# Kernel optimization log

Hardware: AMD Instinct MI355X
Metric: run time of the kernel (lower is better)

## Reference

```python
import jax, jax.numpy as jnp
import numpy as np

N = 100000   # nodes
E = 800000   # edges
H = 256      # hidden_dim == input_dim
L = 3        # num_layers
G = 64       # graphs in batch


def setup_inputs() -> dict:
    key = jax.random.key(0)
    ks = jax.random.split(key, 16)
    s = 0.05
    inp = {
        'x': jax.random.normal(ks[0], (N, H), jnp.float32),
        'edge_index': jax.random.randint(ks[1], (2, E), 0, N, dtype=jnp.int32),
        'batch': jnp.sort(jax.random.randint(ks[2], (N,), 0, G, dtype=jnp.int32)),
        'Ws': jax.random.normal(ks[3], (L, H, H), jnp.float32) * s,
        'Wn': jax.random.normal(ks[4], (L, H, H), jnp.float32) * s,
        'bs': jnp.zeros((L, H), jnp.float32),
        'att_w': jax.random.normal(ks[5], (H, 1), jnp.float32) * s,
        'att_b': jnp.zeros((1,), jnp.float32),
        'ne_W1': jax.random.normal(ks[6], (H, H // 2), jnp.float32) * s,
        'ne_b1': jnp.zeros((H // 2,), jnp.float32),
        'ne_W2': jax.random.normal(ks[7], (H // 2, 1), jnp.float32) * s,
        'ne_b2': jnp.zeros((1,), jnp.float32),
        'nd_W1': jax.random.normal(ks[8], (H, H // 2), jnp.float32) * s,
        'nd_b1': jnp.zeros((H // 2,), jnp.float32),
        'nd_W2': jax.random.normal(ks[9], (H // 2, 1), jnp.float32) * s,
        'nd_b2': jnp.zeros((1,), jnp.float32),
    }
    return inp


def reference(x, edge_index, batch, Ws, Wn, bs, att_w, att_b,
              ne_W1, ne_b1, ne_W2, ne_b2, nd_W1, nd_b1, nd_W2, nd_b2):
    src, dst = edge_index[0], edge_index[1]
    n = x.shape[0]
    # in-degree for mean aggregation (clamped to avoid div-by-zero)
    deg = jax.ops.segment_sum(jnp.ones(src.shape[0], x.dtype), dst, num_segments=n)
    deg = jnp.maximum(deg, 1.0)[:, None]                    # [N,1]
    # GNN encoder: SAGE-mean layers, ReLU (dropout identity at eval)
    h = x
    for l in range(Ws.shape[0]):
        msg = jax.ops.segment_sum(h[src], dst, num_segments=n) / deg  # [N,H]
        h = jax.nn.relu(h @ Ws[l] + msg @ Wn[l] + bs[l])
    # attention pooling: per-graph softmax over node scores
    s = (h @ att_w + att_b)[:, 0]                           # [N]
    m = jax.ops.segment_max(s, batch, num_segments=G)
    e = jnp.exp(s - m[batch])
    denom = jax.ops.segment_sum(e, batch, num_segments=G)
    alpha = (e / denom[batch])[:, None]                     # [N,1]
    g = jax.ops.segment_sum(alpha * h, batch, num_segments=G)  # [G,H]
    # heads: Linear-ReLU-(Dropout)-Linear
    graph_logits = jax.nn.relu(g @ ne_W1 + ne_b1) @ ne_W2 + ne_b2  # [G,1]
    node_logits = jax.nn.relu(h @ nd_W1 + nd_b1) @ nd_W2 + nd_b2  # [N,1]
    return (graph_logits, node_logits)
```

## Files before the change

kernel.cpp:

```cpp
#include <hip/hip_runtime.h>
#include <hip/hip_bf16.h>

#define HID 256
#define HHALF 128

typedef unsigned short u16;
typedef __attribute__((ext_vector_type(8))) short bf16x8;
typedef __attribute__((ext_vector_type(4))) float f32x4;

__device__ __forceinline__ float bf2f(unsigned int u) {
    unsigned int x = (u & 0xffffu) << 16;
    union { unsigned int i; float f; } c; c.i = x; return c.f;
}
__device__ __forceinline__ float lof(unsigned u) {
    union { unsigned i; float f; } c; c.i = u << 16; return c.f;
}
__device__ __forceinline__ float hif(unsigned u) {
    union { unsigned i; float f; } c; c.i = u & 0xffff0000u; return c.f;
}
__device__ __forceinline__ u16 f2bf(float f) {
    __hip_bfloat16 h = __float2bfloat16(f);
    union { __hip_bfloat16 h; u16 u; } c; c.h = h; return c.u;
}

__device__ __forceinline__ void gload16(const u16* g, u16* l) {
    __builtin_amdgcn_global_load_lds(
        (const __attribute__((address_space(1))) void*)g,
        (__attribute__((address_space(3))) void*)l, 16, 0, 0);
}

__device__ __forceinline__ int lbound(const int* __restrict__ a, int n, int key) {
    int lo = 0, hi = n;
    while (lo < hi) {
        int mid = (lo + hi) >> 1;
        if (a[mid] < key) lo = mid + 1; else hi = mid;
    }
    return lo;
}

__global__ void k_count(const int* __restrict__ dst, int* __restrict__ cnt, int E) {
    int i = blockIdx.x * blockDim.x + threadIdx.x;
    if (i < E) atomicAdd(&cnt[dst[i]], 1);
}

__global__ void k_scan_block(const int* __restrict__ cnt, int* __restrict__ bsum, int n) {
    __shared__ int sd[256];
    int tid = threadIdx.x;
    int i = blockIdx.x * 256 + tid;
    int v = (i < n) ? cnt[i] : 0;
    sd[tid] = v; __syncthreads();
    for (int s = 128; s > 0; s >>= 1) {
        if (tid < s) sd[tid] += sd[tid + s];
        __syncthreads();
    }
    if (tid == 0) bsum[blockIdx.x] = sd[0];
}

__global__ void k_scan_top(int* __restrict__ bsum, int nb) {
    __shared__ int sd[512];
    int t = threadIdx.x;
    int v = (t < nb) ? bsum[t] : 0;
    sd[t] = v; __syncthreads();
    for (int s = 1; s < 512; s <<= 1) {
        int x = (t >= s) ? sd[t - s] : 0;
        __syncthreads();
        sd[t] += x;
        __syncthreads();
    }
    if (t < nb) bsum[t] = sd[t] - v;
}

__global__ void k_scan_down(const int* __restrict__ cnt, const int* __restrict__ boff,
                            int* __restrict__ row_off, int n, int total) {
    __shared__ int sd[256];
    int tid = threadIdx.x;
    int i = blockIdx.x * 256 + tid;
    int v = (i < n) ? cnt[i] : 0;
    sd[tid] = v; __syncthreads();
    for (int s = 1; s < 256; s <<= 1) {
        int x = (tid >= s) ? sd[tid - s] : 0;
        __syncthreads();
        sd[tid] += x;
        __syncthreads();
    }
    if (i < n) row_off[i] = boff[blockIdx.x] + sd[tid] - v;
    if (i == 0) row_off[n] = total;
}

__global__ void k_scatter(const int* __restrict__ src, const int* __restrict__ dst,
                          const int* __restrict__ row_off, int* __restrict__ cnt,
                          int* __restrict__ col, int E) {
    int i = blockIdx.x * blockDim.x + threadIdx.x;
    if (i < E) {
        int d = dst[i];
        int p = atomicSub(&cnt[d], 1) - 1;
        col[row_off[d] + p] = src[i];
    }
}

__global__ void k_prep(const float* __restrict__ x, u16* __restrict__ xb, int xtotal4,
                       const float* __restrict__ Ws, const float* __restrict__ Wn,
                       const float* __restrict__ ndW1,
                       u16* __restrict__ WsT, u16* __restrict__ WnT,
                       u16* __restrict__ ndW1T, int L) {
    int idx = blockIdx.x * 256 + threadIdx.x;
    if (idx < xtotal4) {
        float4 v = *(const float4*)&x[(size_t)idx * 4];
        uint2 p;
        p.x = (unsigned)f2bf(v.x) | ((unsigned)f2bf(v.y) << 16);
        p.y = (unsigned)f2bf(v.z) | ((unsigned)f2bf(v.w) << 16);
        *(uint2*)&xb[(size_t)idx * 4] = p;
        return;
    }
    int widx = idx - xtotal4;
    int mat = widx >> 16;
    if (mat >= 2 * L + 1) return;
    int r = widx & 65535;
    int k = r >> 8, c = r & 255;
    if (mat < L) {
        WsT[(size_t)mat * 65536 + c * 256 + k] = f2bf(Ws[(size_t)mat * 65536 + k * 256 + c]);
    } else if (mat < 2 * L) {
        int l = mat - L;
        WnT[(size_t)l * 65536 + c * 256 + k] = f2bf(Wn[(size_t)l * 65536 + k * 256 + c]);
    } else {
        if (c < HHALF) ndW1T[c * 256 + k] = f2bf(ndW1[k * HHALF + c]);
    }
}

__global__ __launch_bounds__(256) void k_agg(
    const u16* __restrict__ h, const int* __restrict__ row_off,
    const int* __restrict__ col, u16* __restrict__ msg, int n) {
    int node = blockIdx.x * 4 + (threadIdx.x >> 6);
    if (node >= n) return;
    int lane = threadIdx.x & 63;
    int half = lane >> 5;
    int t = lane & 31;
    int s0 = row_off[node], s1 = row_off[node + 1];
    float a0 = 0.f, a1 = 0.f, a2 = 0.f, a3 = 0.f;
    float a4 = 0.f, a5 = 0.f, a6 = 0.f, a7 = 0.f;
    int e = s0;
    for (; e + 8 <= s1; e += 8) {
        int c0 = col[e + half];
        int c1 = col[e + 2 + half];
        int c2 = col[e + 4 + half];
        int c3 = col[e + 6 + half];
        uint4 v0 = *(const uint4*)&h[(size_t)c0 * HID + t * 8];
        uint4 v1 = *(const uint4*)&h[(size_t)c1 * HID + t * 8];
        uint4 v2 = *(const uint4*)&h[(size_t)c2 * HID + t * 8];
        uint4 v3 = *(const uint4*)&h[(size_t)c3 * HID + t * 8];
        a0 += (lof(v0.x) + lof(v1.x)) + (lof(v2.x) + lof(v3.x));
        a1 += (hif(v0.x) + hif(v1.x)) + (hif(v2.x) + hif(v3.x));
        a2 += (lof(v0.y) + lof(v1.y)) + (lof(v2.y) + lof(v3.y));
        a3 += (hif(v0.y) + hif(v1.y)) + (hif(v2.y) + hif(v3.y));
        a4 += (lof(v0.z) + lof(v1.z)) + (lof(v2.z) + lof(v3.z));
        a5 += (hif(v0.z) + hif(v1.z)) + (hif(v2.z) + hif(v3.z));
        a6 += (lof(v0.w) + lof(v1.w)) + (lof(v2.w) + lof(v3.w));
        a7 += (hif(v0.w) + hif(v1.w)) + (hif(v2.w) + hif(v3.w));
    }
    if (e < s1) {
        int i0 = e + half, i1 = e + 2 + half, i2 = e + 4 + half, i3 = e + 6 + half;
        float w0 = (i0 < s1) ? 1.f : 0.f; int c0 = col[(i0 < s1) ? i0 : s0];
        float w1 = (i1 < s1) ? 1.f : 0.f; int c1 = col[(i1 < s1) ? i1 : s0];
        float w2 = (i2 < s1) ? 1.f : 0.f; int c2 = col[(i2 < s1) ? i2 : s0];
        float w3 = (i3 < s1) ? 1.f : 0.f; int c3 = col[(i3 < s1) ? i3 : s0];
        uint4 v0 = *(const uint4*)&h[(size_t)c0 * HID + t * 8];
        uint4 v1 = *(const uint4*)&h[(size_t)c1 * HID + t * 8];
        uint4 v2 = *(const uint4*)&h[(size_t)c2 * HID + t * 8];
        uint4 v3 = *(const uint4*)&h[(size_t)c3 * HID + t * 8];
        a0 = fmaf(w0, lof(v0.x), fmaf(w1, lof(v1.x), fmaf(w2, lof(v2.x), fmaf(w3, lof(v3.x), a0))));
        a1 = fmaf(w0, hif(v0.x), fmaf(w1, hif(v1.x), fmaf(w2, hif(v2.x), fmaf(w3, hif(v3.x), a1))));
        a2 = fmaf(w0, lof(v0.y), fmaf(w1, lof(v1.y), fmaf(w2, lof(v2.y), fmaf(w3, lof(v3.y), a2))));
        a3 = fmaf(w0, hif(v0.y), fmaf(w1, hif(v1.y), fmaf(w2, hif(v2.y), fmaf(w3, hif(v3.y), a3))));
        a4 = fmaf(w0, lof(v0.z), fmaf(w1, lof(v1.z), fmaf(w2, lof(v2.z), fmaf(w3, lof(v3.z), a4))));
        a5 = fmaf(w0, hif(v0.z), fmaf(w1, hif(v1.z), fmaf(w2, hif(v2.z), fmaf(w3, hif(v3.z), a5))));
        a6 = fmaf(w0, lof(v0.w), fmaf(w1, lof(v1.w), fmaf(w2, lof(v2.w), fmaf(w3, lof(v3.w), a6))));
        a7 = fmaf(w0, hif(v0.w), fmaf(w1, hif(v1.w), fmaf(w2, hif(v2.w), fmaf(w3, hif(v3.w), a7))));
    }
    a0 += __shfl_xor(a0, 32); a1 += __shfl_xor(a1, 32);
    a2 += __shfl_xor(a2, 32); a3 += __shfl_xor(a3, 32);
    a4 += __shfl_xor(a4, 32); a5 += __shfl_xor(a5, 32);
    a6 += __shfl_xor(a6, 32); a7 += __shfl_xor(a7, 32);
    if (half == 0) {
        int deg = s1 - s0;
        float inv = 1.0f / (float)(deg > 1 ? deg : 1);
        uint4 o;
        o.x = (unsigned)f2bf(a0 * inv) | ((unsigned)f2bf(a1 * inv) << 16);
        o.y = (unsigned)f2bf(a2 * inv) | ((unsigned)f2bf(a3 * inv) << 16);
        o.z = (unsigned)f2bf(a4 * inv) | ((unsigned)f2bf(a5 * inv) << 16);
        o.w = (unsigned)f2bf(a6 * inv) | ((unsigned)f2bf(a7 * inv) << 16);
        *(uint4*)&msg[(size_t)node * HID + t * 8] = o;
    }
}

__global__ __launch_bounds__(512) void k_gemm_bf(
    const u16* __restrict__ A1, const u16* __restrict__ W1t,
    const u16* __restrict__ A2, const u16* __restrict__ W2t,
    const float* __restrict__ bias, u16* __restrict__ out,
    int n, int ncols,
    const float* __restrict__ dotw, const float* __restrict__ dotb,
    float* __restrict__ dotout) {
    __shared__ __align__(16) u16 As[128 * 64];
    __shared__ __align__(16) u16 Bs[256 * 64];
    const int tid  = threadIdx.x;
    const int lane = tid & 63;
    const int w    = tid >> 6;
    const int wr   = w >> 2, wc = w & 3;
    const int brow = blockIdx.x * 128;
    const int nkt  = A2 ? 8 : 4;

    f32x4 acc[4][4];
    #pragma unroll
    for (int m = 0; m < 4; ++m)
        #pragma unroll
        for (int q = 0; q < 4; ++q)
            acc[m][q] = (f32x4){0.f, 0.f, 0.f, 0.f};

    const int as0 = tid, as1 = tid + 512;
    int ar0 = brow + (as0 >> 3); if (ar0 >= n) ar0 = n - 1;
    int ar1 = brow + (as1 >> 3); if (ar1 >= n) ar1 = n - 1;
    const size_t asrc0 = (size_t)ar0 * HID + (size_t)(((as0 & 7) ^ (((as0 >> 3) >> 1) & 7)) * 8);
    const size_t asrc1 = (size_t)ar1 * HID + (size_t)(((as1 & 7) ^ (((as1 >> 3) >> 1) & 7)) * 8);
    u16* adst0 = &As[(w * 64) * 8];
    u16* adst1 = &As[(512 + w * 64) * 8];

    size_t bsrc[4];
    u16*   bdst[4];
    #pragma unroll
    for (int i = 0; i < 4; ++i) {
        int s = tid + i * 512;
        int row = s >> 3;
        bsrc[i] = (size_t)row * HID + (size_t)(((s & 7) ^ ((row >> 1) & 7)) * 8);
        bdst[i] = &Bs[(i * 512 + w * 64) * 8];
    }

    const int lr = lane & 15;
    const int lq = lane >> 4;
    const int swz = (lr >> 1) & 7;

    for (int kt = 0; kt < nkt; ++kt) {
        const u16* A = (kt < 4) ? A1 : A2;
        const u16* W = (kt < 4) ? W1t : W2t;
        const int k0 = (kt & 3) * 64;
        __syncthreads();
        gload16(A + asrc0 + k0, adst0);
        gload16(A + asrc1 + k0, adst1);
        gload16(W + bsrc[0] + k0, bdst[0]);
        gload16(W + bsrc[1] + k0, bdst[1]);
        gload16(W + bsrc[2] + k0, bdst[2]);
        gload16(W + bsrc[3] + k0, bdst[3]);
        __syncthreads();
        #pragma unroll
        for (int ks = 0; ks < 2; ++ks) {
            const int ch = (ks * 4 + lq) ^ swz;
            bf16x8 af[4], bg[4];
            #pragma unroll
            for (int m = 0; m < 4; ++m)
                af[m] = *(const bf16x8*)&As[(wr * 64 + m * 16 + lr) * 64 + ch * 8];
            #pragma unroll
            for (int q = 0; q < 4; ++q)
                bg[q] = *(const bf16x8*)&Bs[(wc * 64 + q * 16 + lr) * 64 + ch * 8];
            #pragma unroll
            for (int m = 0; m < 4; ++m)
                #pragma unroll
                for (int q = 0; q < 4; ++q)
                    acc[m][q] = __builtin_amdgcn_mfma_f32_16x16x32_bf16(
                        bg[q], af[m], acc[m][q], 0, 0, 0);
        }
    }

    if (dotout) __syncthreads();
    float* dred = (float*)As;
    #pragma unroll
    for (int m = 0; m < 4; ++m) {
        int row = brow + wr * 64 + m * 16 + lr;
        bool rok = row < n;
        float dpart = 0.f;
        #pragma unroll
        for (int q = 0; q < 4; ++q) {
            int col = wc * 64 + q * 16 + lq * 4;
            if (col < ncols) {
                float4 bb = *(const float4*)&bias[col];
                float r0 = fmaxf(acc[m][q][0] + bb.x, 0.f);
                float r1 = fmaxf(acc[m][q][1] + bb.y, 0.f);
                float r2 = fmaxf(acc[m][q][2] + bb.z, 0.f);
                float r3 = fmaxf(acc[m][q][3] + bb.w, 0.f);
                if (out && rok) {
                    uint2 o;
                    o.x = (unsigned)f2bf(r0) | ((unsigned)f2bf(r1) << 16);
                    o.y = (unsigned)f2bf(r2) | ((unsigned)f2bf(r3) << 16);
                    *(uint2*)&out[(size_t)row * ncols + col] = o;
                }
                if (dotout) {
                    float4 wv = *(const float4*)&dotw[col];
                    dpart += r0 * wv.x + r1 * wv.y + r2 * wv.z + r3 * wv.w;
                }
            }
        }
        if (dotout) {
            dpart += __shfl_xor(dpart, 16);
            dpart += __shfl_xor(dpart, 32);
            if (lane < 16) dred[(wr * 64 + m * 16 + lane) * 4 + wc] = dpart;
        }
    }
    if (dotout) {
        __syncthreads();
        if (tid < 128) {
            int row = brow + tid;
            if (row < n) {
                float s = (dred[tid * 4 + 0] + dred[tid * 4 + 1])
                        + (dred[tid * 4 + 2] + dred[tid * 4 + 3]);
                dotout[row] = s + dotb[0];
            }
        }
    }
}

__global__ __launch_bounds__(256) void k_ndhead(
    const u16* __restrict__ A1, const u16* __restrict__ W1t,
    const float* __restrict__ bias, int n,
    const float* __restrict__ dotw, const float* __restrict__ dotb,
    float* __restrict__ dotout) {
    __shared__ __align__(16) u16 As[128 * 64];
    __shared__ __align__(16) u16 Bs[128 * 64];
    const int tid  = threadIdx.x;
    const int lane = tid & 63;
    const int w    = tid >> 6;
    const int wr   = w >> 1, wc = w & 1;
    const int brow = blockIdx.x * 128;

    f32x4 acc[4][4];
    #pragma unroll
    for (int m = 0; m < 4; ++m)
        #pragma unroll
        for (int q = 0; q < 4; ++q)
            acc[m][q] = (f32x4){0.f, 0.f, 0.f, 0.f};

    size_t asrc[4], bsrc[4];
    u16 *adst[4], *bdst[4];
    #pragma unroll
    for (int i = 0; i < 4; ++i) {
        int s = tid + i * 256;
        int row = s >> 3;
        int ch = ((s & 7) ^ ((row >> 1) & 7)) * 8;
        int ar = brow + row; if (ar >= n) ar = n - 1;
        asrc[i] = (size_t)ar * HID + ch;
        bsrc[i] = (size_t)row * HID + ch;
        adst[i] = &As[(i * 256 + w * 64) * 8];
        bdst[i] = &Bs[(i * 256 + w * 64) * 8];
    }

    const int lr = lane & 15;
    const int lq = lane >> 4;
    const int swz = (lr >> 1) & 7;

    for (int kt = 0; kt < 4; ++kt) {
        const int k0 = kt * 64;
        __syncthreads();
        #pragma unroll
        for (int i = 0; i < 4; ++i) gload16(A1 + asrc[i] + k0, adst[i]);
        #pragma unroll
        for (int i = 0; i < 4; ++i) gload16(W1t + bsrc[i] + k0, bdst[i]);
        __syncthreads();
        #pragma unroll
        for (int ks = 0; ks < 2; ++ks) {
            const int ch = (ks * 4 + lq) ^ swz;
            bf16x8 af[4], bg[4];
            #pragma unroll
            for (int m = 0; m < 4; ++m)
                af[m] = *(const bf16x8*)&As[(wr * 64 + m * 16 + lr) * 64 + ch * 8];
            #pragma unroll
            for (int q = 0; q < 4; ++q)
                bg[q] = *(const bf16x8*)&Bs[(wc * 64 + q * 16 + lr) * 64 + ch * 8];
            #pragma unroll
            for (int m = 0; m < 4; ++m)
                #pragma unroll
                for (int q = 0; q < 4; ++q)
                    acc[m][q] = __builtin_amdgcn_mfma_f32_16x16x32_bf16(
                        bg[q], af[m], acc[m][q], 0, 0, 0);
        }
    }

    __syncthreads();
    float* dred = (float*)As;
    #pragma unroll
    for (int m = 0; m < 4; ++m) {
        float dpart = 0.f;
        #pragma unroll
        for (int q = 0; q < 4; ++q) {
            int col = wc * 64 + q * 16 + lq * 4;
            float4 bb = *(const float4*)&bias[col];
            float4 wv = *(const float4*)&dotw[col];
            dpart += fmaxf(acc[m][q][0] + bb.x, 0.f) * wv.x
                   + fmaxf(acc[m][q][1] + bb.y, 0.f) * wv.y
                   + fmaxf(acc[m][q][2] + bb.z, 0.f) * wv.z
                   + fmaxf(acc[m][q][3] + bb.w, 0.f) * wv.w;
        }
        dpart += __shfl_xor(dpart, 16);
        dpart += __shfl_xor(dpart, 32);
        if (lane < 16) dred[(wr * 64 + m * 16 + lane) * 2 + wc] = dpart;
    }
    __syncthreads();
    if (tid < 128) {
        int row = brow + tid;
        if (row < n) dotout[row] = dred[tid * 2 + 0] + dred[tid * 2 + 1] + dotb[0];
    }
}

__global__ void k_mdenom(const float* __restrict__ s, const int* __restrict__ batch,
                         int n, float* __restrict__ m, float* __restrict__ denom) {
    int g = blockIdx.x;
    int t = threadIdx.x;
    int i0 = lbound(batch, n, g);
    int i1 = lbound(batch, n, g + 1);
    __shared__ float red[256];
    float mx = -INFINITY;
    for (int i = i0 + t; i < i1; i += 256) mx = fmaxf(mx, s[i]);
    red[t] = mx; __syncthreads();
    for (int st = 128; st; st >>= 1) {
        if (t < st) red[t] = fmaxf(red[t], red[t + st]);
        __syncthreads();
    }
    float gm = red[0];
    __syncthreads();
    float sm = 0.f;
    for (int i = i0 + t; i < i1; i += 256) sm += expf(s[i] - gm);
    red[t] = sm; __syncthreads();
    for (int st = 128; st; st >>= 1) {
        if (t < st) red[t] += red[t + st];
        __syncthreads();
    }
    if (t == 0) { m[g] = gm; denom[g] = red[0]; }
}

__global__ void k_pool(const u16* __restrict__ h, const float* __restrict__ sarr,
                       const float* __restrict__ marr, const float* __restrict__ denom,
                       const int* __restrict__ batch, int n, int G,
                       float* __restrict__ gpool16) {
    int g = blockIdx.x, sp = blockIdx.y, t = threadIdx.x;
    int i0 = lbound(batch, n, g);
    int i1 = lbound(batch, n, g + 1);
    int len = i1 - i0;
    int a = i0 + (int)((long long)len * sp / 16);
    int b = i0 + (int)((long long)len * (sp + 1) / 16);
    float dn = denom[g];
    float inv = (dn > 0.f) ? 1.0f / dn : 0.f;
    float mg = marr[g];
    float acc = 0.f;
    for (int i = a; i < b; ++i)
        acc += expf(sarr[i] - mg) * inv * bf2f(h[(size_t)i * HID + t]);
    gpool16[((size_t)sp * G + g) * HID + t] = acc;
}

__global__ void k_ghead(const float* __restrict__ gpool16, int G,
                        const float* __restrict__ W1, const float* __restrict__ b1,
                        const float* __restrict__ W2, const float* __restrict__ b2,
                        float* __restrict__ out) {
    int g = blockIdx.x, t = threadIdx.x;
    __shared__ float row[HID];
    __shared__ float red[128];
    float v0 = 0.f, v1 = 0.f;
    for (int sp = 0; sp < 16; ++sp) {
        const float* p = gpool16 + ((size_t)sp * G + g) * HID;
        v0 += p[t];
        v1 += p[t + 128];
    }
    row[t] = v0;
    row[t + 128] = v1;
    __syncthreads();
    float acc = 0.f;
    #pragma unroll 8
    for (int k = 0; k < HID; ++k) acc = fmaf(row[k], W1[k * HHALF + t], acc);
    float hid = fmaxf(acc + b1[t], 0.f);
    red[t] = hid * W2[t];
    __syncthreads();
    for (int st = 64; st; st >>= 1) {
        if (t < st) red[t] += red[t + st];
        __syncthreads();
    }
    if (t == 0) out[g] = red[0] + b2[0];
}

extern "C" void kernel_launch(void* const* d_in, const int* in_sizes, int n_in,
                              void* d_out, int out_size, void* d_ws, size_t ws_size,
                              hipStream_t stream) {
    const float* x      = (const float*)d_in[0];
    const int*   eidx   = (const int*)d_in[1];
    const int*   batch  = (const int*)d_in[2];
    const float* Ws     = (const float*)d_in[3];
    const float* Wn     = (const float*)d_in[4];
    const float* bs     = (const float*)d_in[5];
    const float* att_w  = (const float*)d_in[6];
    const float* att_b  = (const float*)d_in[7];
    const float* ne_W1  = (const float*)d_in[8];
    const float* ne_b1  = (const float*)d_in[9];
    const float* ne_W2  = (const float*)d_in[10];
    const float* ne_b2  = (const float*)d_in[11];
    const float* nd_W1  = (const float*)d_in[12];
    const float* nd_b1  = (const float*)d_in[13];
    const float* nd_W2  = (const float*)d_in[14];
    const float* nd_b2  = (const float*)d_in[15];
    float* out = (float*)d_out;

    const int N = in_sizes[2];
    const int E = in_sizes[1] / 2;
    const int L = in_sizes[3] / (HID * HID);
    const int G = out_size - N;

    const int* src = eidx;
    const int* dst = eidx + E;

    size_t off = 0;
    auto alloc = [&](size_t bytes) {
        void* p = (char*)d_ws + off;
        off += (bytes + 255) & ~(size_t)255;
        return p;
    };
    int*   cnt     = (int*)alloc((size_t)N * 4);
    int*   row_off = (int*)alloc((size_t)(N + 1) * 4);
    int*   col     = (int*)alloc((size_t)E * 4);
    int*   bsum    = (int*)alloc(1024 * 4);
    float* sarr    = (float*)alloc((size_t)N * 4);
    float* marr    = (float*)alloc((size_t)G * 4);
    float* denom   = (float*)alloc((size_t)G * 4);
    float* gpool16 = (float*)alloc((size_t)16 * G * HID * 4);
    u16*   xb      = (u16*)alloc((size_t)N * HID * 2);
    u16*   msgb    = (u16*)alloc((size_t)N * HID * 2);
    u16*   hb1     = (u16*)alloc((size_t)N * HID * 2);
    u16*   hb2     = (u16*)alloc((size_t)N * HID * 2);
    u16*   WsT     = (u16*)alloc((size_t)L * HID * HID * 2);
    u16*   WnT     = (u16*)alloc((size_t)L * HID * HID * 2);
    u16*   ndW1T   = (u16*)alloc((size_t)HID * HID * 2);
    (void)ws_size;

    const int eb = (E + 255) / 256;
    const int nb = (N + 255) / 256;

    hipMemsetAsync(cnt, 0, (size_t)N * 4, stream);
    k_count<<<eb, 256, 0, stream>>>(dst, cnt, E);
    k_scan_block<<<nb, 256, 0, stream>>>(cnt, bsum, N);
    k_scan_top<<<1, 512, 0, stream>>>(bsum, nb);
    k_scan_down<<<nb, 256, 0, stream>>>(cnt, bsum, row_off, N, E);
    k_scatter<<<eb, 256, 0, stream>>>(src, dst, row_off, cnt, col, E);

    const int xtotal4 = N * HID / 4;
    const int prep_blocks = (xtotal4 + 255) / 256 + (2 * L + 1) * (HID * HID / 256);
    k_prep<<<prep_blocks, 256, 0, stream>>>(
        x, xb, xtotal4, Ws, Wn, nd_W1, WsT, WnT, ndW1T, L);

    const int gx = (N + 127) / 128;
    const u16* hin = xb;
    u16* hout = hb1;
    for (int l = 0; l < L; ++l) {
        bool last = (l == L - 1);
        k_agg<<<(N + 3) / 4, 256, 0, stream>>>(hin, row_off, col, msgb, N);
        k_gemm_bf<<<gx, 512, 0, stream>>>(
            hin, WsT + (size_t)l * HID * HID, msgb, WnT + (size_t)l * HID * HID,
            bs + (size_t)l * HID, hout, N, HID,
            last ? att_w : nullptr, last ? att_b : nullptr, last ? sarr : nullptr);
        hin = hout;
        hout = (hout == hb1) ? hb2 : hb1;
    }
    const u16* h = hin;

    k_mdenom<<<G, 256, 0, stream>>>(sarr, batch, N, marr, denom);
    k_pool<<<dim3(G, 16), HID, 0, stream>>>(h, sarr, marr, denom, batch, N, G, gpool16);

    k_ghead<<<G, HHALF, 0, stream>>>(gpool16, G, ne_W1, ne_b1, ne_W2, ne_b2, out);

    k_ndhead<<<gx, 256, 0, stream>>>(
        h, ndW1T, nd_b1, N, nd_W2, nd_b2, out + G);
}
```

Baseline: 532.0 us.

## Merge CSR build, prep, and attention pooling stages into cooperative kernels

Replaces the memset, count, three scan kernels, scatter and prep kernels with one cooperative kernel that uses grid-wide syncs between phases. It also merges the softmax max/denominator, pooling and graph head kernels into a second cooperative kernel. The aim is to cut launch overhead and the gaps between many small kernels. In exchange, the grids are limited in size (1024 blocks for prep, G*16 for attention), grid.sync adds its own cost, and the bandwidth-heavy x conversion now runs through a grid-stride loop.

```diff
diff --git a/kernel.cpp b/kernel.cpp
--- a/kernel.cpp
+++ b/kernel.cpp
@@ -1,5 +1,8 @@
 #include <hip/hip_runtime.h>
 #include <hip/hip_bf16.h>
+#include <hip/hip_cooperative_groups.h>
+
+namespace cg = cooperative_groups;
 
 #define HID 256
 #define HHALF 128
@@ -38,92 +41,97 @@
     return lo;
 }
 
-__global__ void k_count(const int* __restrict__ dst, int* __restrict__ cnt, int E) {
-    int i = blockIdx.x * blockDim.x + threadIdx.x;
-    if (i < E) atomicAdd(&cnt[dst[i]], 1);
-}
-
-__global__ void k_scan_block(const int* __restrict__ cnt, int* __restrict__ bsum, int n) {
-    __shared__ int sd[256];
-    int tid = threadIdx.x;
-    int i = blockIdx.x * 256 + tid;
-    int v = (i < n) ? cnt[i] : 0;
-    sd[tid] = v; __syncthreads();
-    for (int s = 128; s > 0; s >>= 1) {
-        if (tid < s) sd[tid] += sd[tid + s];
-        __syncthreads();
-    }
-    if (tid == 0) bsum[blockIdx.x] = sd[0];
-}
-
-__global__ void k_scan_top(int* __restrict__ bsum, int nb) {
+__global__ __launch_bounds__(256) void k_csr_prep(
+    const int* __restrict__ src, const int* __restrict__ dst,
+    int* __restrict__ cnt, int* __restrict__ bsum,
+    int* __restrict__ row_off, int* __restrict__ col,
+    int N, int E, int nb,
+    const float* __restrict__ x, u16* __restrict__ xb, int xtotal4,
+    const float* __restrict__ Ws, const float* __restrict__ Wn,
+    const float* __restrict__ ndW1,
+    u16* __restrict__ WsT, u16* __restrict__ WnT,
+    u16* __restrict__ ndW1T, int L) {
+    cg::grid_group grid = cg::this_grid();
     __shared__ int sd[512];
-    int t = threadIdx.x;
-    int v = (t < nb) ? bsum[t] : 0;
-    sd[t] = v; __syncthreads();
-    for (int s = 1; s < 512; s <<= 1) {
-        int x = (t >= s) ? sd[t - s] : 0;
-        __syncthreads();
-        sd[t] += x;
-        __syncthreads();
-    }
-    if (t < nb) bsum[t] = sd[t] - v;
-}
-
-__global__ void k_scan_down(const int* __restrict__ cnt, const int* __restrict__ boff,
-                            int* __restrict__ row_off, int n, int total) {
-    __shared__ int sd[256];
-    int tid = threadIdx.x;
-    int i = blockIdx.x * 256 + tid;
-    int v = (i < n) ? cnt[i] : 0;
-    sd[tid] = v; __syncthreads();
-    for (int s = 1; s < 256; s <<= 1) {
-        int x = (tid >= s) ? sd[tid - s] : 0;
-        __syncthreads();
-        sd[tid] += x;
-        __syncthreads();
-    }
-    if (i < n) row_off[i] = boff[blockIdx.x] + sd[tid] - v;
-    if (i == 0) row_off[n] = total;
-}
-
-__global__ void k_scatter(const int* __restrict__ src, const int* __restrict__ dst,
-                          const int* __restrict__ row_off, int* __restrict__ cnt,
-                          int* __restrict__ col, int E) {
-    int i = blockIdx.x * blockDim.x + threadIdx.x;
-    if (i < E) {
+    const int t   = threadIdx.x;
+    const int gid = blockIdx.x * 256 + t;
+    const int gsz = gridDim.x * 256;
+
+    for (int i = gid; i < N; i += gsz) cnt[i] = 0;
+    grid.sync();
+
+    for (int i = gid; i < E; i += gsz) atomicAdd(&cnt[dst[i]], 1);
+    for (int i = gid; i < xtotal4; i += gsz) {
+        float4 v = *(const float4*)&x[(size_t)i * 4];
+        uint2 p;
+        p.x = (unsigned)f2bf(v.x) | ((unsigned)f2bf(v.y) << 16);
+        p.y = (unsigned)f2bf(v.z) | ((unsigned)f2bf(v.w) << 16);
+        *(uint2*)&xb[(size_t)i * 4] = p;
+    }
+    const int wtotal = (2 * L + 1) * 65536;
+    for (int i = gid; i < wtotal; i += gsz) {
+        int mat = i >> 16;
+        int r = i & 65535;
+        int k = r >> 8, c = r & 255;
+        if (mat < L) {
+            WsT[(size_t)mat * 65536 + c * 256 + k] = f2bf(Ws[(size_t)mat * 65536 + k * 256 + c]);
+        } else if (mat < 2 * L) {
+            int l = mat - L;
+            WnT[(size_t)l * 65536 + c * 256 + k] = f2bf(Wn[(size_t)l * 65536 + k * 256 + c]);
+        } else {
+            if (c < HHALF) ndW1T[c * 256 + k] = f2bf(ndW1[k * HHALF + c]);
+        }
+    }
+    grid.sync();
+
+    if (blockIdx.x < (unsigned)nb) {
+        int i = blockIdx.x * 256 + t;
+        int v = (i < N) ? cnt[i] : 0;
+        sd[t] = v; __syncthreads();
+        for (int s = 128; s > 0; s >>= 1) {
+            if (t < s) sd[t] += sd[t + s];
+            __syncthreads();
+        }
+        if (t == 0) bsum[blockIdx.x] = sd[0];
+    }
+    grid.sync();
+
+    if (blockIdx.x == 0) {
+        int v0 = (t < nb) ? bsum[t] : 0;
+        int v1 = (t + 256 < nb) ? bsum[t + 256] : 0;
+        sd[t] = v0; sd[t + 256] = v1;
+        __syncthreads();
+        for (int s = 1; s < 512; s <<= 1) {
+            int x0 = (t >= s) ? sd[t - s] : 0;
+            int x1 = (t + 256 >= s) ? sd[t + 256 - s] : 0;
+            __syncthreads();
+            sd[t] += x0; sd[t + 256] += x1;
+            __syncthreads();
+        }
+        if (t < nb) bsum[t] = sd[t] - v0;
+        if (t + 256 < nb) bsum[t + 256] = sd[t + 256] - v1;
+    }
+    grid.sync();
+
+    if (blockIdx.x < (unsigned)nb) {
+        int i = blockIdx.x * 256 + t;
+        int v = (i < N) ? cnt[i] : 0;
+        sd[t] = v; __syncthreads();
+        for (int s = 1; s < 256; s <<= 1) {
+            int xx = (t >= s) ? sd[t - s] : 0;
+            __syncthreads();
+            sd[t] += xx;
+            __syncthreads();
+        }
+        if (i < N) row_off[i] = bsum[blockIdx.x] + sd[t] - v;
+        if (gid == 0) row_off[N] = E;
+    }
+    grid.sync();
+
+    for (int i = gid; i < E; i += gsz) {
         int d = dst[i];
         int p = atomicSub(&cnt[d], 1) - 1;
         col[row_off[d] + p] = src[i];
-    }
-}
-
-__global__ void k_prep(const float* __restrict__ x, u16* __restrict__ xb, int xtotal4,
-                       const float* __restrict__ Ws, const float* __restrict__ Wn,
-                       const float* __restrict__ ndW1,
-                       u16* __restrict__ WsT, u16* __restrict__ WnT,
-                       u16* __restrict__ ndW1T, int L) {
-    int idx = blockIdx.x * 256 + threadIdx.x;
-    if (idx < xtotal4) {
-        float4 v = *(const float4*)&x[(size_t)idx * 4];
-        uint2 p;
-        p.x = (unsigned)f2bf(v.x) | ((unsigned)f2bf(v.y) << 16);
-        p.y = (unsigned)f2bf(v.z) | ((unsigned)f2bf(v.w) << 16);
-        *(uint2*)&xb[(size_t)idx * 4] = p;
-        return;
-    }
-    int widx = idx - xtotal4;
-    int mat = widx >> 16;
-    if (mat >= 2 * L + 1) return;
-    int r = widx & 65535;
-    int k = r >> 8, c = r & 255;
-    if (mat < L) {
-        WsT[(size_t)mat * 65536 + c * 256 + k] = f2bf(Ws[(size_t)mat * 65536 + k * 256 + c]);
-    } else if (mat < 2 * L) {
-        int l = mat - L;
-        WnT[(size_t)l * 65536 + c * 256 + k] = f2bf(Wn[(size_t)l * 65536 + k * 256 + c]);
-    } else {
-        if (c < HHALF) ndW1T[c * 256 + k] = f2bf(ndW1[k * HHALF + c]);
     }
 }
 
@@ -406,78 +414,78 @@
     }
 }
 
-__global__ void k_mdenom(const float* __restrict__ s, const int* __restrict__ batch,
-                         int n, float* __restrict__ m, float* __restrict__ denom) {
-    int g = blockIdx.x;
-    int t = threadIdx.x;
-    int i0 = lbound(batch, n, g);
-    int i1 = lbound(batch, n, g + 1);
+__global__ __launch_bounds__(256) void k_attn(
+    const u16* __restrict__ h, const float* __restrict__ sarr,
+    const int* __restrict__ batch, int n, int G,
+    float* __restrict__ marr, float* __restrict__ denom, float* __restrict__ gpool16,
+    const float* __restrict__ W1, const float* __restrict__ b1,
+    const float* __restrict__ W2, const float* __restrict__ b2,
+    float* __restrict__ out) {
+    cg::grid_group grid = cg::this_grid();
+    const int b = blockIdx.x, t = threadIdx.x;
+    const int g = b >> 4, sp = b & 15;
     __shared__ float red[256];
-    float mx = -INFINITY;
-    for (int i = i0 + t; i < i1; i += 256) mx = fmaxf(mx, s[i]);
-    red[t] = mx; __syncthreads();
-    for (int st = 128; st; st >>= 1) {
-        if (t < st) red[t] = fmaxf(red[t], red[t + st]);
-        __syncthreads();
-    }
-    float gm = red[0];
-    __syncthreads();
-    float sm = 0.f;
-    for (int i = i0 + t; i < i1; i += 256) sm += expf(s[i] - gm);
-    red[t] = sm; __syncthreads();
-    for (int st = 128; st; st >>= 1) {
-        if (t < st) red[t] += red[t + st];
-        __syncthreads();
-    }
-    if (t == 0) { m[g] = gm; denom[g] = red[0]; }
-}
-
-__global__ void k_pool(const u16* __restrict__ h, const float* __restrict__ sarr,
-                       const float* __restrict__ marr, const float* __restrict__ denom,
-                       const int* __restrict__ batch, int n, int G,
-                       float* __restrict__ gpool16) {
-    int g = blockIdx.x, sp = blockIdx.y, t = threadIdx.x;
-    int i0 = lbound(batch, n, g);
-    int i1 = lbound(batch, n, g + 1);
-    int len = i1 - i0;
-    int a = i0 + (int)((long long)len * sp / 16);
-    int b = i0 + (int)((long long)len * (sp + 1) / 16);
-    float dn = denom[g];
-    float inv = (dn > 0.f) ? 1.0f / dn : 0.f;
-    float mg = marr[g];
-    float acc = 0.f;
-    for (int i = a; i < b; ++i)
-        acc += expf(sarr[i] - mg) * inv * bf2f(h[(size_t)i * HID + t]);
-    gpool16[((size_t)sp * G + g) * HID + t] = acc;
-}
-
-__global__ void k_ghead(const float* __restrict__ gpool16, int G,
-                        const float* __restrict__ W1, const float* __restrict__ b1,
-                        const float* __restrict__ W2, const float* __restrict__ b2,
-                        float* __restrict__ out) {
-    int g = blockIdx.x, t = threadIdx.x;
     __shared__ float row[HID];
-    __shared__ float red[128];
-    float v0 = 0.f, v1 = 0.f;
-    for (int sp = 0; sp < 16; ++sp) {
-        const float* p = gpool16 + ((size_t)sp * G + g) * HID;
-        v0 += p[t];
-        v1 += p[t + 128];
-    }
-    row[t] = v0;
-    row[t + 128] = v1;
-    __syncthreads();
-    float acc = 0.f;
-    #pragma unroll 8
-    for (int k = 0; k < HID; ++k) acc = fmaf(row[k], W1[k * HHALF + t], acc);
-    float hid = fmaxf(acc + b1[t], 0.f);
-    red[t] = hid * W2[t];
-    __syncthreads();
-    for (int st = 64; st; st >>= 1) {
-        if (t < st) red[t] += red[t + st];
-        __syncthreads();
-    }
-    if (t == 0) out[g] = red[0] + b2[0];
+
+    if (sp == 0) {
+        int i0 = lbound(batch, n, g);
+        int i1 = lbound(batch, n, g + 1);
+        float mx = -INFINITY;
+        for (int i = i0 + t; i < i1; i += 256) mx = fmaxf(mx, sarr[i]);
+        red[t] = mx; __syncthreads();
+        for (int st = 128; st; st >>= 1) {
+            if (t < st) red[t] = fmaxf(red[t], red[t + st]);
+            __syncthreads();
+        }
+        float gm = red[0];
+        __syncthreads();
+        float sm = 0.f;
+        for (int i = i0 + t; i < i1; i += 256) sm += expf(sarr[i] - gm);
+        red[t] = sm; __syncthreads();
+        for (int st = 128; st; st >>= 1) {
+            if (t < st) red[t] += red[t + st];
+            __syncthreads();
+        }
+        if (t == 0) { marr[g] = gm; denom[g] = red[0]; }
+    }
+    grid.sync();
+
+    {
+        int i0 = lbound(batch, n, g);
+        int i1 = lbound(batch, n, g + 1);
+        int len = i1 - i0;
+        int a  = i0 + (int)((long long)len * sp / 16);
+        int bb = i0 + (int)((long long)len * (sp + 1) / 16);
+        float dn = denom[g];
+        float inv = (dn > 0.f) ? 1.0f / dn : 0.f;
+        float mg = marr[g];
+        float acc = 0.f;
+        for (int i = a; i < bb; ++i)
+            acc += expf(sarr[i] - mg) * inv * bf2f(h[(size_t)i * HID + t]);
+        gpool16[((size_t)sp * G + g) * HID + t] = acc;
+    }
+    grid.sync();
+
+    if (b < G) {
+        float v = 0.f;
+        for (int s2 = 0; s2 < 16; ++s2)
+            v += gpool16[((size_t)s2 * G + b) * HID + t];
+        row[t] = v;
+        __syncthreads();
+        if (t < HHALF) {
+            float acc = 0.f;
+            #pragma unroll 8
+            for (int k = 0; k < HID; ++k) acc = fmaf(row[k], W1[k * HHALF + t], acc);
+            float hid = fmaxf(acc + b1[t], 0.f);
+            red[t] = hid * W2[t];
+        }
+        __syncthreads();
+        for (int st = 64; st; st >>= 1) {
+            if (t < st) red[t] += red[t + st];
+            __syncthreads();
+        }
+        if (t == 0) out[b] = red[0] + b2[0];
+    }
 }
 
 extern "C" void kernel_launch(void* const* d_in, const int* in_sizes, int n_in,
@@ -501,10 +509,10 @@
     const float* nd_b2  = (const float*)d_in[15];
     float* out = (float*)d_out;
 
-    const int N = in_sizes[2];
-    const int E = in_sizes[1] / 2;
-    const int L = in_sizes[3] / (HID * HID);
-    const int G = out_size - N;
+    int N = in_sizes[2];
+    int E = in_sizes[1] / 2;
+    int L = in_sizes[3] / (HID * HID);
+    int G = out_size - N;
 
     const int* src = eidx;
     const int* dst = eidx + E;
@@ -532,20 +540,19 @@
     u16*   ndW1T   = (u16*)alloc((size_t)HID * HID * 2);
     (void)ws_size;
 
-    const int eb = (E + 255) / 256;
-    const int nb = (N + 255) / 256;
-
-    hipMemsetAsync(cnt, 0, (size_t)N * 4, stream);
-    k_count<<<eb, 256, 0, stream>>>(dst, cnt, E);
-    k_scan_block<<<nb, 256, 0, stream>>>(cnt, bsum, N);
-    k_scan_top<<<1, 512, 0, stream>>>(bsum, nb);
-    k_scan_down<<<nb, 256, 0, stream>>>(cnt, bsum, row_off, N, E);
-    k_scatter<<<eb, 256, 0, stream>>>(src, dst, row_off, cnt, col, E);
-
-    const int xtotal4 = N * HID / 4;
-    const int prep_blocks = (xtotal4 + 255) / 256 + (2 * L + 1) * (HID * HID / 256);
-    k_prep<<<prep_blocks, 256, 0, stream>>>(
-        x, xb, xtotal4, Ws, Wn, nd_W1, WsT, WnT, ndW1T, L);
+    int nb = (N + 255) / 256;
+    int xtotal4 = N * HID / 4;
+
+    {
+        void* cargs[] = {
+            (void*)&src, (void*)&dst, (void*)&cnt, (void*)&bsum,
+            (void*)&row_off, (void*)&col, (void*)&N, (void*)&E, (void*)&nb,
+            (void*)&x, (void*)&xb, (void*)&xtotal4,
+            (void*)&Ws, (void*)&Wn, (void*)&nd_W1,
+            (void*)&WsT, (void*)&WnT, (void*)&ndW1T, (void*)&L };
+        hipLaunchCooperativeKernel((void*)k_csr_prep, dim3(1024), dim3(256),
+                                   cargs, 0, stream);
+    }
 
     const int gx = (N + 127) / 128;
     const u16* hin = xb;
@@ -562,11 +569,16 @@
     }
     const u16* h = hin;
 
-    k_mdenom<<<G, 256, 0, stream>>>(sarr, batch, N, marr, denom);
-    k_pool<<<dim3(G, 16), HID, 0, stream>>>(h, sarr, marr, denom, batch, N, G, gpool16);
-
-    k_ghead<<<G, HHALF, 0, stream>>>(gpool16, G, ne_W1, ne_b1, ne_W2, ne_b2, out);
-
     k_ndhead<<<gx, 256, 0, stream>>>(
         h, ndW1T, nd_b1, N, nd_W2, nd_b2, out + G);
-}
+
+    {
+        void* aargs[] = {
+            (void*)&h, (void*)&sarr, (void*)&batch, (void*)&N, (void*)&G,
+            (void*)&marr, (void*)&denom, (void*)&gpool16,
+            (void*)&ne_W1, (void*)&ne_b1, (void*)&ne_W2, (void*)&ne_b2,
+            (void*)&out };
+        hipLaunchCooperativeKernel((void*)k_attn, dim3(G * 16), dim3(256),
+                                   aargs, 0, stream);
+    }
+}
```

After: 1.260 ms. 2.37x slower.
